# Optimization experiments

Hardware: AMD Instinct MI355X
Metric: run time of the kernel (lower is better)

## Reference

```python
import jax, jax.numpy as jnp
import numpy as np

B, N, NF, H = 16, 128, 128, 128


def setup_inputs() -> dict:
    key = jax.random.key(0)
    ks = jax.random.split(key, 10)
    s = lambda k, sh: jax.random.normal(k, sh, dtype=jnp.float32) * (1.0 / np.sqrt(sh[0]))
    return {
        "node_feat": jax.random.normal(ks[0], (B, N, NF), dtype=jnp.float32),
        "pos": jax.random.normal(ks[1], (B, N, 3), dtype=jnp.float32),
        "valid": jnp.ones((B, N), dtype=jnp.float32),
        "adj": jax.random.uniform(ks[2], (B, N, N), dtype=jnp.float32),
        "We1": s(ks[3], (2 * NF + 2, H)),
        "We2": s(ks[4], (H, H)),
        "Wc1": s(ks[5], (H, H)),
        "Wc2": s(ks[6], (H, 1)),
        "Wn1": s(ks[7], (NF + H, H)),
        "Wn2": s(ks[8], (H, NF)),
        "Wi": s(ks[9], (H, 1)),
    }


def reference(node_feat, pos, valid, adj, We1, We2, Wc1, Wc2, Wn1, Wn2, Wi):
    silu = jax.nn.silu
    n = node_feat.shape[1]
    # all-pairs broadcast features [B,N,N,NF]
    hi = jnp.broadcast_to(node_feat[:, :, None, :], (B, n, n, NF))
    hj = jnp.broadcast_to(node_feat[:, None, :, :], (B, n, n, NF))
    vec = pos[:, :, None, :] - pos[:, None, :, :]            # [B,N,N,3]
    dist = jnp.sum(vec * vec, axis=-1, keepdims=True)        # [B,N,N,1]
    adj4 = adj[..., None]                                    # [B,N,N,1]
    edge_input = jnp.concatenate([hi, hj, dist, adj4], axis=-1)
    m_ij = silu(silu(edge_input @ We1) @ We2)                # [B,N,N,H]
    # normalized direction vectors
    norm = jnp.linalg.norm(vec, axis=-1, keepdims=True)
    vecn = vec / jnp.maximum(norm, 1e-10)
    # pairwise valid mask [B,N,N,1]
    vmask = (valid[:, :, None] * valid[:, None, :])[..., None]
    # coordinate update
    C = (1.0 / (jnp.sum(valid, axis=-1) - 1.0))[:, None, None]
    phi_x = silu(m_ij @ Wc1) @ Wc2                           # [B,N,N,1]
    pos_new = pos + C * jnp.sum(vecn * phi_x * vmask, axis=2)
    # inference gating
    e_ij = jax.nn.sigmoid(m_ij @ Wi)
    m_ij = m_ij * e_ij
    # masked message aggregation over j
    message = jnp.sum(m_ij * adj4, axis=2)                   # [B,N,H]
    node_input = jnp.concatenate([node_feat, message], axis=-1)
    node_new = node_feat + silu(node_input @ Wn1) @ Wn2
    return node_new, pos_new
```

## Files before the change

### kernel.cpp

```cpp
#include <hip/hip_runtime.h>
#include <hip/hip_bf16.h>

#define B_  16
#define N_  128
#define NF_ 128
#define H_  128

typedef __attribute__((ext_vector_type(8))) short short8;
typedef __attribute__((ext_vector_type(4))) float floatx4;

__device__ __forceinline__ float silu_f(float x) {
    return x * __builtin_amdgcn_rcpf(1.0f + __expf(-x));
}
__device__ __forceinline__ float sigm_f(float x) {
    return __builtin_amdgcn_rcpf(1.0f + __expf(-x));
}
__device__ __forceinline__ unsigned short f2bf(float x) {
    union { float f; unsigned u; } v; v.f = x;
    unsigned r = (v.u + 0x7FFFu + ((v.u >> 16) & 1u)) >> 16;
    return (unsigned short)r;
}
__device__ __forceinline__ short f2bf_fast(float x) {
    union { __hip_bfloat16 h; short s; } u;
    u.h = __float2bfloat16(x);
    return u.s;
}
__device__ __forceinline__ float bf2f(unsigned short s) {
    union { unsigned u; float f; } v; v.u = ((unsigned)s) << 16;
    return v.f;
}

__global__ __launch_bounds__(128) void k1_pre(const float* __restrict__ nf,
                                              const float* __restrict__ We1,
                                              float* __restrict__ A_ws,
                                              float* __restrict__ Bm_ws) {
    const int b  = blockIdx.x >> 4;
    const int r0 = (blockIdx.x & 15) << 3;
    const int h  = threadIdx.x;
    __shared__ float rows[8][128];
#pragma unroll
    for (int r = 0; r < 8; ++r)
        rows[r][h] = nf[((size_t)(b * N_ + r0 + r)) * NF_ + h];
    __syncthreads();
    float a[8], bm[8];
#pragma unroll
    for (int r = 0; r < 8; ++r) { a[r] = 0.f; bm[r] = 0.f; }
    for (int c = 0; c < NF_; ++c) {
        const float w1 = We1[c * H_ + h];
        const float w2 = We1[(NF_ + c) * H_ + h];
#pragma unroll
        for (int r = 0; r < 8; ++r) {
            const float x = rows[r][c];
            a[r]  = fmaf(x, w1, a[r]);
            bm[r] = fmaf(x, w2, bm[r]);
        }
    }
#pragma unroll
    for (int r = 0; r < 8; ++r) {
        A_ws [((size_t)(b * N_ + r0 + r)) * H_ + h] = a[r];
        Bm_ws[((size_t)(b * N_ + r0 + r)) * H_ + h] = bm[r];
    }
}

__global__ __launch_bounds__(64) void kC(const float* __restrict__ valid,
                                         float* __restrict__ Cinv) {
    const int b = blockIdx.x;
    const int t = threadIdx.x;
    float v = valid[b * N_ + t] + valid[b * N_ + 64 + t];
#pragma unroll
    for (int m = 32; m >= 1; m >>= 1) v += __shfl_down(v, m, 64);
    if (t == 0) Cinv[b] = 1.0f / (v - 1.0f);
}

#define OFF_BM    0
#define OFF_W2T   34816
#define OFF_WC1X  69632
#define OFF_MB    108800
#define OFF_AW    143616
#define OFF_WAB   145792
#define OFF_WC2   146336
#define OFF_POSJ  146848
#define OFF_VALJ  148384
#define OFF_POSI  148896
#define OFF_VALI  149024
#define SMEM_K2   149088

__global__ __launch_bounds__(512, 2) void k2_edge(
        const float* __restrict__ pos,
        const float* __restrict__ valid,
        const float* __restrict__ adj,
        const float* __restrict__ We1,
        const float* __restrict__ We2,
        const float* __restrict__ Wc1,
        const float* __restrict__ Wc2,
        const float* __restrict__ Wi,
        const float* __restrict__ A_ws,
        const float* __restrict__ Bm_ws,
        const float* __restrict__ Cinv,
        float* __restrict__ msg_ws,
        float* __restrict__ pos_out) {
    __shared__ __align__(16) char smem[SMEM_K2];
    unsigned short* BM   = (unsigned short*)(smem + OFF_BM);
    unsigned short* W2T  = (unsigned short*)(smem + OFF_W2T);
    unsigned short* WC1X = (unsigned short*)(smem + OFF_WC1X);
    unsigned short* MB   = (unsigned short*)(smem + OFF_MB);
    unsigned short* AW   = (unsigned short*)(smem + OFF_AW);
    unsigned short* WAB  = (unsigned short*)(smem + OFF_WAB);
    float* wc2s = (float*)(smem + OFF_WC2);
    float* posj = (float*)(smem + OFF_POSJ);
    float* valj = (float*)(smem + OFF_VALJ);
    float* posi = (float*)(smem + OFF_POSI);
    float* vali = (float*)(smem + OFF_VALI);

    const int tid = threadIdx.x;
    const int b   = blockIdx.x >> 4;
    const int i0  = (blockIdx.x & 15) << 3;

    for (int q = tid; q < (N_ * H_) / 4; q += 512) {
        const int j  = q >> 5;
        const int ch = (q << 2) & 127;
        const float4 v = *(const float4*)(Bm_ws + ((size_t)(b * N_ + j)) * H_ + ch);
        ushort4 o;
        o.x = f2bf(v.x); o.y = f2bf(v.y); o.z = f2bf(v.z); o.w = f2bf(v.w);
        *(ushort4*)(BM + j * 136 + ch) = o;
    }
    for (int x = tid; x < H_ * H_; x += 512) {
        const int k = x >> 7, n = x & 127;
        W2T[n * 136 + k] = f2bf(We2[x]);
    }
    for (int x = tid; x < H_ * H_; x += 512) {
        const int k = x >> 7, n = x & 127;
        WC1X[n * 136 + k] = f2bf(Wc1[x]);
    }
    if (tid < 128) WC1X[128 * 136 + tid] = f2bf(Wi[tid]);
    for (int x = tid; x < 15 * 136; x += 512)
        WC1X[129 * 136 + x] = 0;
    for (int x = tid; x < 8 * H_; x += 512)
        AW[(x >> 7) * 136 + (x & 127)] =
            f2bf(A_ws[((size_t)(b * N_ + i0 + (x >> 7))) * H_ + (x & 127)]);
    if (tid < 256)
        WAB[(tid >> 7) * 136 + (tid & 127)] = f2bf(We1[(256 + (tid >> 7)) * H_ + (tid & 127)]);
    if (tid < 128) {
        wc2s[tid] = Wc2[tid];
        valj[tid] = valid[b * N_ + tid];
    }
    if (tid >= 128) posj[tid - 128] = pos[b * N_ * 3 + (tid - 128)];
    if (tid < 24)   posi[tid] = pos[b * N_ * 3 + i0 * 3 + tid];
    if (tid >= 32 && tid < 40) vali[tid - 32] = valid[b * N_ + i0 + (tid - 32)];
    __syncthreads();

    const int w  = tid >> 6;
    const int l  = tid & 63;
    const int lr = l & 15;
    const int lg = l >> 4;
    const int i  = i0 + w;
    unsigned short* MBs = MB + w * (16 * 136);

    float wc2v[8];
#pragma unroll
    for (int nt = 0; nt < 8; ++nt) wc2v[nt] = wc2s[nt * 16 + lr];
    const float vi   = vali[w];
    const float pix  = posi[w * 3 + 0], piy = posi[w * 3 + 1], piz = posi[w * 3 + 2];
    const float cinv = Cinv[b];

    float msg[8] = {0.f, 0.f, 0.f, 0.f, 0.f, 0.f, 0.f, 0.f};
    float px = 0.f, py = 0.f, pz = 0.f;
    const floatx4 zf = {0.f, 0.f, 0.f, 0.f};

    for (int jc = 0; jc < 8; ++jc) {
        const int jj = jc * 16 + lr;
        const float adjv = adj[((size_t)(b * N_ + i)) * N_ + jj];
        const float vj   = valj[jj];
        const float vx = pix - posj[jj * 3 + 0];
        const float vy = piy - posj[jj * 3 + 1];
        const float vz = piz - posj[jj * 3 + 2];
        const float dist = vx * vx + vy * vy + vz * vz;
        const float vm   = vi * vj;
        const float rn   = __builtin_amdgcn_rcpf(fmaxf(sqrtf(dist), 1e-10f));
        const float vnx = vx * rn, vny = vy * rn, vnz = vz * rn;

        short8 af[4];
#pragma unroll
        for (int ks = 0; ks < 4; ++ks) {
            const int co = ks * 32 + lg * 8;
            const short8 bm8 = *(const short8*)(BM + jj * 136 + co);
            const short8 aw8 = *(const short8*)(AW + w * 136 + co);
            const short8 wa8 = *(const short8*)(WAB + co);
            const short8 wb8 = *(const short8*)(WAB + 136 + co);
#pragma unroll
            for (int e = 0; e < 8; ++e) {
                const float pre = bf2f((unsigned short)aw8[e])
                                + bf2f((unsigned short)bm8[e])
                                + dist * bf2f((unsigned short)wa8[e])
                                + adjv * bf2f((unsigned short)wb8[e]);
                af[ks][e] = f2bf_fast(silu_f(pre));
            }
        }
        floatx4 acc1[8];
#pragma unroll
        for (int nt = 0; nt < 8; ++nt) acc1[nt] = zf;
#pragma unroll
        for (int nt = 0; nt < 8; ++nt)
#pragma unroll
            for (int ks = 0; ks < 4; ++ks) {
                const short8 bf = *(const short8*)(W2T + (nt * 16 + lr) * 136 + ks * 32 + lg * 8);
                acc1[nt] = __builtin_amdgcn_mfma_f32_16x16x32_bf16(af[ks], bf, acc1[nt], 0, 0, 0);
            }
#pragma unroll
        for (int nt = 0; nt < 8; ++nt)
#pragma unroll
            for (int r = 0; r < 4; ++r)
                acc1[nt][r] = silu_f(acc1[nt][r]);

#pragma unroll
        for (int nt = 0; nt < 8; ++nt)
#pragma unroll
            for (int r = 0; r < 4; ++r)
                MBs[(lg * 4 + r) * 136 + nt * 16 + lr] = (unsigned short)f2bf_fast(acc1[nt][r]);
        short8 af2[4];
#pragma unroll
        for (int ks = 0; ks < 4; ++ks)
            af2[ks] = *(const short8*)(MBs + lr * 136 + ks * 32 + lg * 8);

        floatx4 accg = zf;
#pragma unroll
        for (int ks = 0; ks < 4; ++ks) {
            const short8 bf = *(const short8*)(WC1X + (8 * 16 + lr) * 136 + ks * 32 + lg * 8);
            accg = __builtin_amdgcn_mfma_f32_16x16x32_bf16(af2[ks], bf, accg, 0, 0, 0);
        }
        float t4[4];
#pragma unroll
        for (int r = 0; r < 4; ++r) {
            const float ep  = __shfl(accg[r], l & 48);
            const float ajr = __shfl(adjv, (l & 48) | (lg * 4 + r));
            t4[r] = sigm_f(ep) * ajr;
        }
#pragma unroll
        for (int nt = 0; nt < 8; ++nt)
            msg[nt] += acc1[nt][0] * t4[0] + acc1[nt][1] * t4[1]
                     + acc1[nt][2] * t4[2] + acc1[nt][3] * t4[3];

        float ph[4] = {0.f, 0.f, 0.f, 0.f};
#pragma unroll
        for (int nt = 0; nt < 8; ++nt) {
            floatx4 acc2 = zf;
#pragma unroll
            for (int ks = 0; ks < 4; ++ks) {
                const short8 bf = *(const short8*)(WC1X + (nt * 16 + lr) * 136 + ks * 32 + lg * 8);
                acc2 = __builtin_amdgcn_mfma_f32_16x16x32_bf16(af2[ks], bf, acc2, 0, 0, 0);
            }
#pragma unroll
            for (int r = 0; r < 4; ++r)
                ph[r] = fmaf(silu_f(acc2[r]), wc2v[nt], ph[r]);
        }
#pragma unroll
        for (int msk = 1; msk <= 8; msk <<= 1)
#pragma unroll
            for (int r = 0; r < 4; ++r)
                ph[r] += __shfl_xor(ph[r], msk);
        const int src = ((lr >> 2) << 4) | lr;
        const float q0 = __shfl(ph[0], src), q1 = __shfl(ph[1], src);
        const float q2 = __shfl(ph[2], src), q3 = __shfl(ph[3], src);
        const int rr = lr & 3;
        const float phl = rr == 0 ? q0 : rr == 1 ? q1 : rr == 2 ? q2 : q3;
        const float pm = phl * vm;
        px = fmaf(vnx, pm, px); py = fmaf(vny, pm, py); pz = fmaf(vnz, pm, pz);
    }

#pragma unroll
    for (int msk = 16; msk <= 32; msk <<= 1)
#pragma unroll
        for (int nt = 0; nt < 8; ++nt)
            msg[nt] += __shfl_xor(msg[nt], msk);
    if (l < 16) {
#pragma unroll
        for (int nt = 0; nt < 8; ++nt)
            msg_ws[((size_t)(b * N_ + i)) * H_ + nt * 16 + l] = msg[nt];
    }
#pragma unroll
    for (int msk = 1; msk <= 8; msk <<= 1) {
        px += __shfl_xor(px, msk);
        py += __shfl_xor(py, msk);
        pz += __shfl_xor(pz, msk);
    }
    if (l == 0) {
        const size_t o = ((size_t)(b * N_ + i)) * 3;
        pos_out[o + 0] = pos[o + 0] + cinv * px;
        pos_out[o + 1] = pos[o + 1] + cinv * py;
        pos_out[o + 2] = pos[o + 2] + cinv * pz;
    }
}

__global__ __launch_bounds__(128) void k3_node(
        const float* __restrict__ nf,
        const float* __restrict__ Wn1,
        const float* __restrict__ Wn2,
        const float* __restrict__ msg_ws,
        float* __restrict__ out) {
    const int b  = blockIdx.x >> 4;
    const int r0 = (blockIdx.x & 15) << 3;
    const int h  = threadIdx.x;
    __shared__ float in_s[8][256];
    __shared__ float t_s[8][128];
#pragma unroll
    for (int r = 0; r < 8; ++r) {
        in_s[r][h]       = nf[((size_t)(b * N_ + r0 + r)) * NF_ + h];
        in_s[r][128 + h] = msg_ws[((size_t)(b * N_ + r0 + r)) * H_ + h];
    }
    __syncthreads();
    float acc[8];
#pragma unroll
    for (int r = 0; r < 8; ++r) acc[r] = 0.f;
    for (int c = 0; c < 256; ++c) {
        const float wv = Wn1[c * H_ + h];
#pragma unroll
        for (int r = 0; r < 8; ++r) acc[r] = fmaf(in_s[r][c], wv, acc[r]);
    }
#pragma unroll
    for (int r = 0; r < 8; ++r) t_s[r][h] = silu_f(acc[r]);
    __syncthreads();
    float o[8];
#pragma unroll
    for (int r = 0; r < 8; ++r) o[r] = 0.f;
    for (int c = 0; c < 128; ++c) {
        const float wv = Wn2[c * NF_ + h];
#pragma unroll
        for (int r = 0; r < 8; ++r) o[r] = fmaf(t_s[r][c], wv, o[r]);
    }
#pragma unroll
    for (int r = 0; r < 8; ++r)
        out[((size_t)(b * N_ + r0 + r)) * NF_ + h] = in_s[r][h] + o[r];
}

extern "C" void kernel_launch(void* const* d_in, const int* in_sizes, int n_in,
                              void* d_out, int out_size, void* d_ws, size_t ws_size,
                              hipStream_t stream) {
    const float* node_feat = (const float*)d_in[0];
    const float* pos   = (const float*)d_in[1];
    const float* valid = (const float*)d_in[2];
    const float* adj   = (const float*)d_in[3];
    const float* We1   = (const float*)d_in[4];
    const float* We2   = (const float*)d_in[5];
    const float* Wc1   = (const float*)d_in[6];
    const float* Wc2   = (const float*)d_in[7];
    const float* Wn1   = (const float*)d_in[8];
    const float* Wn2   = (const float*)d_in[9];
    const float* Wi    = (const float*)d_in[10];

    float* out     = (float*)d_out;
    float* pos_out = out + (size_t)B_ * N_ * NF_;

    const size_t node_elems = (size_t)B_ * N_ * H_;
    if (ws_size < (3 * node_elems + B_) * sizeof(float)) return;
    float* A_ws   = (float*)d_ws;
    float* Bm_ws  = A_ws + node_elems;
    float* msg_ws = Bm_ws + node_elems;
    float* Cinv   = msg_ws + node_elems;

    k1_pre<<<B_ * 16, 128, 0, stream>>>(node_feat, We1, A_ws, Bm_ws);
    kC<<<B_, 64, 0, stream>>>(valid, Cinv);
    k2_edge<<<B_ * 16, 512, 0, stream>>>(pos, valid, adj, We1, We2, Wc1, Wc2, Wi,
                                         A_ws, Bm_ws, Cinv, msg_ws, pos_out);
    k3_node<<<B_ * 16, 128, 0, stream>>>(node_feat, Wn1, Wn2, msg_ws, out);
}
```

Baseline: 82.78 us.

## Shrink edge-kernel LDS with XOR swizzle, bf16 Bm from global, scalar gate

k1 now writes Bm directly as bf16, and k2 reads it from global memory instead of staging a padded copy in LDS. The weight tiles switch from padded rows to an XOR-swizzled layout, and the per-wave scratch buffer is cut to one 16x32 slice. The Wi gate is computed with a cross-lane reduction instead of an extra MFMA column. Together these shrink LDS from about 149KB to 80KB, so launch bounds can ask for 4 blocks per CU instead of 2. The cost is global-memory loads of Bm in the inner loop and tighter register limits.

```diff
diff --git a/kernel.cpp b/kernel.cpp
--- a/kernel.cpp
+++ b/kernel.cpp
@@ -33,7 +33,7 @@
 __global__ __launch_bounds__(128) void k1_pre(const float* __restrict__ nf,
                                               const float* __restrict__ We1,
                                               float* __restrict__ A_ws,
-                                              float* __restrict__ Bm_ws) {
+                                              unsigned short* __restrict__ Bmh) {
     const int b  = blockIdx.x >> 4;
     const int r0 = (blockIdx.x & 15) << 3;
     const int h  = threadIdx.x;
@@ -57,8 +57,8 @@
     }
 #pragma unroll
     for (int r = 0; r < 8; ++r) {
-        A_ws [((size_t)(b * N_ + r0 + r)) * H_ + h] = a[r];
-        Bm_ws[((size_t)(b * N_ + r0 + r)) * H_ + h] = bm[r];
+        A_ws[((size_t)(b * N_ + r0 + r)) * H_ + h] = a[r];
+        Bmh [((size_t)(b * N_ + r0 + r)) * H_ + h] = f2bf(bm[r]);
     }
 }
 
@@ -72,20 +72,20 @@
     if (t == 0) Cinv[b] = 1.0f / (v - 1.0f);
 }
 
-#define OFF_BM    0
-#define OFF_W2T   34816
-#define OFF_WC1X  69632
-#define OFF_MB    108800
-#define OFF_AW    143616
-#define OFF_WAB   145792
-#define OFF_WC2   146336
-#define OFF_POSJ  146848
-#define OFF_VALJ  148384
-#define OFF_POSI  148896
-#define OFF_VALI  149024
-#define SMEM_K2   149088
-
-__global__ __launch_bounds__(512, 2) void k2_edge(
+#define OFF_W2T   0
+#define OFF_WC1T  32768
+#define OFF_MB    65536
+#define OFF_AW    73728
+#define OFF_WAB   75776
+#define OFF_WC2   76288
+#define OFF_WIS   76800
+#define OFF_POSJ  77312
+#define OFF_VALJ  78848
+#define OFF_POSI  79360
+#define OFF_VALI  79488
+#define SMEM_K2   79552
+
+__global__ __launch_bounds__(512, 4) void k2_edge(
         const float* __restrict__ pos,
         const float* __restrict__ valid,
         const float* __restrict__ adj,
@@ -95,18 +95,18 @@
         const float* __restrict__ Wc2,
         const float* __restrict__ Wi,
         const float* __restrict__ A_ws,
-        const float* __restrict__ Bm_ws,
+        const unsigned short* __restrict__ Bmh,
         const float* __restrict__ Cinv,
         float* __restrict__ msg_ws,
         float* __restrict__ pos_out) {
     __shared__ __align__(16) char smem[SMEM_K2];
-    unsigned short* BM   = (unsigned short*)(smem + OFF_BM);
-    unsigned short* W2T  = (unsigned short*)(smem + OFF_W2T);
-    unsigned short* WC1X = (unsigned short*)(smem + OFF_WC1X);
-    unsigned short* MB   = (unsigned short*)(smem + OFF_MB);
-    unsigned short* AW   = (unsigned short*)(smem + OFF_AW);
-    unsigned short* WAB  = (unsigned short*)(smem + OFF_WAB);
+    char* W2Tb  = smem + OFF_W2T;
+    char* WC1Tb = smem + OFF_WC1T;
+    unsigned short* MB  = (unsigned short*)(smem + OFF_MB);
+    unsigned short* AW  = (unsigned short*)(smem + OFF_AW);
+    unsigned short* WAB = (unsigned short*)(smem + OFF_WAB);
     float* wc2s = (float*)(smem + OFF_WC2);
+    float* wis  = (float*)(smem + OFF_WIS);
     float* posj = (float*)(smem + OFF_POSJ);
     float* valj = (float*)(smem + OFF_VALJ);
     float* posi = (float*)(smem + OFF_POSI);
@@ -116,32 +116,22 @@
     const int b   = blockIdx.x >> 4;
     const int i0  = (blockIdx.x & 15) << 3;
 
-    for (int q = tid; q < (N_ * H_) / 4; q += 512) {
-        const int j  = q >> 5;
-        const int ch = (q << 2) & 127;
-        const float4 v = *(const float4*)(Bm_ws + ((size_t)(b * N_ + j)) * H_ + ch);
-        ushort4 o;
-        o.x = f2bf(v.x); o.y = f2bf(v.y); o.z = f2bf(v.z); o.w = f2bf(v.w);
-        *(ushort4*)(BM + j * 136 + ch) = o;
-    }
     for (int x = tid; x < H_ * H_; x += 512) {
         const int k = x >> 7, n = x & 127;
-        W2T[n * 136 + k] = f2bf(We2[x]);
+        *(unsigned short*)(W2Tb + ((n * 256 + k * 2) ^ ((n & 7) << 4))) = f2bf(We2[x]);
     }
     for (int x = tid; x < H_ * H_; x += 512) {
         const int k = x >> 7, n = x & 127;
-        WC1X[n * 136 + k] = f2bf(Wc1[x]);
-    }
-    if (tid < 128) WC1X[128 * 136 + tid] = f2bf(Wi[tid]);
-    for (int x = tid; x < 15 * 136; x += 512)
-        WC1X[129 * 136 + x] = 0;
+        *(unsigned short*)(WC1Tb + ((n * 256 + k * 2) ^ ((n & 7) << 4))) = f2bf(Wc1[x]);
+    }
     for (int x = tid; x < 8 * H_; x += 512)
-        AW[(x >> 7) * 136 + (x & 127)] =
+        AW[(x >> 7) * 128 + (x & 127)] =
             f2bf(A_ws[((size_t)(b * N_ + i0 + (x >> 7))) * H_ + (x & 127)]);
     if (tid < 256)
-        WAB[(tid >> 7) * 136 + (tid & 127)] = f2bf(We1[(256 + (tid >> 7)) * H_ + (tid & 127)]);
+        WAB[(tid >> 7) * 128 + (tid & 127)] = f2bf(We1[(256 + (tid >> 7)) * H_ + (tid & 127)]);
     if (tid < 128) {
         wc2s[tid] = Wc2[tid];
+        wis[tid]  = Wi[tid];
         valj[tid] = valid[b * N_ + tid];
     }
     if (tid >= 128) posj[tid - 128] = pos[b * N_ * 3 + (tid - 128)];
@@ -154,11 +144,13 @@
     const int lr = l & 15;
     const int lg = l >> 4;
     const int i  = i0 + w;
-    unsigned short* MBs = MB + w * (16 * 136);
-
-    float wc2v[8];
-#pragma unroll
-    for (int nt = 0; nt < 8; ++nt) wc2v[nt] = wc2s[nt * 16 + lr];
+    unsigned short* MBq = MB + w * 512;
+
+    const int swv = (lr & 7) << 4;
+    int cs[4];
+#pragma unroll
+    for (int ks = 0; ks < 4; ++ks) cs[ks] = (ks * 64 + lg * 16) ^ swv;
+
     const float vi   = vali[w];
     const float pix  = posi[w * 3 + 0], piy = posi[w * 3 + 1], piz = posi[w * 3 + 2];
     const float cinv = Cinv[b];
@@ -183,10 +175,10 @@
 #pragma unroll
         for (int ks = 0; ks < 4; ++ks) {
             const int co = ks * 32 + lg * 8;
-            const short8 bm8 = *(const short8*)(BM + jj * 136 + co);
-            const short8 aw8 = *(const short8*)(AW + w * 136 + co);
+            const short8 bm8 = *(const short8*)(Bmh + ((size_t)(b * N_ + jj)) * H_ + co);
+            const short8 aw8 = *(const short8*)(AW + w * 128 + co);
             const short8 wa8 = *(const short8*)(WAB + co);
-            const short8 wb8 = *(const short8*)(WAB + 136 + co);
+            const short8 wb8 = *(const short8*)(WAB + 128 + co);
 #pragma unroll
             for (int e = 0; e < 8; ++e) {
                 const float pre = bf2f((unsigned short)aw8[e])
@@ -203,7 +195,7 @@
         for (int nt = 0; nt < 8; ++nt)
 #pragma unroll
             for (int ks = 0; ks < 4; ++ks) {
-                const short8 bf = *(const short8*)(W2T + (nt * 16 + lr) * 136 + ks * 32 + lg * 8);
+                const short8 bf = *(const short8*)(W2Tb + (nt * 16 + lr) * 256 + cs[ks]);
                 acc1[nt] = __builtin_amdgcn_mfma_f32_16x16x32_bf16(af[ks], bf, acc1[nt], 0, 0, 0);
             }
 #pragma unroll
@@ -212,46 +204,57 @@
             for (int r = 0; r < 4; ++r)
                 acc1[nt][r] = silu_f(acc1[nt][r]);
 
-#pragma unroll
-        for (int nt = 0; nt < 8; ++nt)
-#pragma unroll
-            for (int r = 0; r < 4; ++r)
-                MBs[(lg * 4 + r) * 136 + nt * 16 + lr] = (unsigned short)f2bf_fast(acc1[nt][r]);
-        short8 af2[4];
-#pragma unroll
-        for (int ks = 0; ks < 4; ++ks)
-            af2[ks] = *(const short8*)(MBs + lr * 136 + ks * 32 + lg * 8);
-
-        floatx4 accg = zf;
-#pragma unroll
-        for (int ks = 0; ks < 4; ++ks) {
-            const short8 bf = *(const short8*)(WC1X + (8 * 16 + lr) * 136 + ks * 32 + lg * 8);
-            accg = __builtin_amdgcn_mfma_f32_16x16x32_bf16(af2[ks], bf, accg, 0, 0, 0);
-        }
+        float ep[4] = {0.f, 0.f, 0.f, 0.f};
+#pragma unroll
+        for (int nt = 0; nt < 8; ++nt) {
+            const float wv = wis[nt * 16 + lr];
+#pragma unroll
+            for (int r = 0; r < 4; ++r)
+                ep[r] = fmaf(acc1[nt][r], wv, ep[r]);
+        }
+#pragma unroll
+        for (int msk = 1; msk <= 8; msk <<= 1)
+#pragma unroll
+            for (int r = 0; r < 4; ++r)
+                ep[r] += __shfl_xor(ep[r], msk);
         float t4[4];
 #pragma unroll
         for (int r = 0; r < 4; ++r) {
-            const float ep  = __shfl(accg[r], l & 48);
             const float ajr = __shfl(adjv, (l & 48) | (lg * 4 + r));
-            t4[r] = sigm_f(ep) * ajr;
+            t4[r] = sigm_f(ep[r]) * ajr;
         }
 #pragma unroll
         for (int nt = 0; nt < 8; ++nt)
             msg[nt] += acc1[nt][0] * t4[0] + acc1[nt][1] * t4[1]
                      + acc1[nt][2] * t4[2] + acc1[nt][3] * t4[3];
 
+        short8 af2[4];
+#pragma unroll
+        for (int ks = 0; ks < 4; ++ks) {
+#pragma unroll
+            for (int h = 0; h < 2; ++h) {
+                const int nt = 2 * ks + h;
+#pragma unroll
+                for (int r = 0; r < 4; ++r)
+                    MBq[(lg * 4 + r) * 32 + h * 16 + lr] =
+                        (unsigned short)f2bf_fast(acc1[nt][r]);
+            }
+            af2[ks] = *(const short8*)(MBq + lr * 32 + lg * 8);
+        }
+
         float ph[4] = {0.f, 0.f, 0.f, 0.f};
 #pragma unroll
         for (int nt = 0; nt < 8; ++nt) {
             floatx4 acc2 = zf;
 #pragma unroll
             for (int ks = 0; ks < 4; ++ks) {
-                const short8 bf = *(const short8*)(WC1X + (nt * 16 + lr) * 136 + ks * 32 + lg * 8);
+                const short8 bf = *(const short8*)(WC1Tb + (nt * 16 + lr) * 256 + cs[ks]);
                 acc2 = __builtin_amdgcn_mfma_f32_16x16x32_bf16(af2[ks], bf, acc2, 0, 0, 0);
             }
-#pragma unroll
-            for (int r = 0; r < 4; ++r)
-                ph[r] = fmaf(silu_f(acc2[r]), wc2v[nt], ph[r]);
+            const float wv = wc2s[nt * 16 + lr];
+#pragma unroll
+            for (int r = 0; r < 4; ++r)
+                ph[r] = fmaf(silu_f(acc2[r]), wv, ph[r]);
         }
 #pragma unroll
         for (int msk = 1; msk <= 8; msk <<= 1)
@@ -351,15 +354,15 @@
     float* pos_out = out + (size_t)B_ * N_ * NF_;
 
     const size_t node_elems = (size_t)B_ * N_ * H_;
-    if (ws_size < (3 * node_elems + B_) * sizeof(float)) return;
-    float* A_ws   = (float*)d_ws;
-    float* Bm_ws  = A_ws + node_elems;
-    float* msg_ws = Bm_ws + node_elems;
+    if (ws_size < node_elems * 4 + node_elems * 2 + node_elems * 4 + 64) return;
+    float* A_ws = (float*)d_ws;
+    unsigned short* Bmh = (unsigned short*)(A_ws + node_elems);
+    float* msg_ws = (float*)((char*)Bmh + node_elems * 2);
     float* Cinv   = msg_ws + node_elems;
 
-    k1_pre<<<B_ * 16, 128, 0, stream>>>(node_feat, We1, A_ws, Bm_ws);
+    k1_pre<<<B_ * 16, 128, 0, stream>>>(node_feat, We1, A_ws, Bmh);
     kC<<<B_, 64, 0, stream>>>(valid, Cinv);
     k2_edge<<<B_ * 16, 512, 0, stream>>>(pos, valid, adj, We1, We2, Wc1, Wc2, Wi,
-                                         A_ws, Bm_ws, Cinv, msg_ws, pos_out);
+                                         A_ws, Bmh, Cinv, msg_ws, pos_out);
     k3_node<<<B_ * 16, 128, 0, stream>>>(node_feat, Wn1, Wn2, msg_ws, out);
 }
```

Result: slower. 95.65 us (+15.5%).

## Split edge j-loop across two waves per row and shrink staging buffer

Applied to the files above, without the earlier changes.

The edge kernel now launches 1024 threads per block, with two waves per node row each handling half of the j chunks. Partial messages and position updates are combined through shared memory after a block barrier. The per-wave staging buffer is cut to a 16x32 slice that is reused per k-step, which lowers LDS use. This doubles the waves available to hide MFMA and memory latency but adds a reduction step and a barrier, and the launch bounds put heavy pressure on registers.

```diff
diff --git a/kernel.cpp b/kernel.cpp
--- a/kernel.cpp
+++ b/kernel.cpp
@@ -75,17 +75,19 @@
 #define OFF_BM    0
 #define OFF_W2T   34816
 #define OFF_WC1X  69632
-#define OFF_MB    108800
-#define OFF_AW    143616
-#define OFF_WAB   145792
-#define OFF_WC2   146336
-#define OFF_POSJ  146848
-#define OFF_VALJ  148384
-#define OFF_POSI  148896
-#define OFF_VALI  149024
-#define SMEM_K2   149088
-
-__global__ __launch_bounds__(512, 2) void k2_edge(
+#define OFF_MBQ   108800
+#define OFF_AW    125184
+#define OFF_WAB   127360
+#define OFF_WC2   127904
+#define OFF_POSJ  128416
+#define OFF_VALJ  129952
+#define OFF_POSI  130464
+#define OFF_VALI  130592
+#define OFF_MSGC  130656
+#define OFF_POSC  138848
+#define SMEM_K2   139104
+
+__global__ __launch_bounds__(1024, 4) void k2_edge(
         const float* __restrict__ pos,
         const float* __restrict__ valid,
         const float* __restrict__ adj,
@@ -103,7 +105,7 @@
     unsigned short* BM   = (unsigned short*)(smem + OFF_BM);
     unsigned short* W2T  = (unsigned short*)(smem + OFF_W2T);
     unsigned short* WC1X = (unsigned short*)(smem + OFF_WC1X);
-    unsigned short* MB   = (unsigned short*)(smem + OFF_MB);
+    unsigned short* MBQ  = (unsigned short*)(smem + OFF_MBQ);
     unsigned short* AW   = (unsigned short*)(smem + OFF_AW);
     unsigned short* WAB  = (unsigned short*)(smem + OFF_WAB);
     float* wc2s = (float*)(smem + OFF_WC2);
@@ -111,12 +113,14 @@
     float* valj = (float*)(smem + OFF_VALJ);
     float* posi = (float*)(smem + OFF_POSI);
     float* vali = (float*)(smem + OFF_VALI);
+    float* MSGC = (float*)(smem + OFF_MSGC);
+    float* POSC = (float*)(smem + OFF_POSC);
 
     const int tid = threadIdx.x;
     const int b   = blockIdx.x >> 4;
     const int i0  = (blockIdx.x & 15) << 3;
 
-    for (int q = tid; q < (N_ * H_) / 4; q += 512) {
+    for (int q = tid; q < (N_ * H_) / 4; q += 1024) {
         const int j  = q >> 5;
         const int ch = (q << 2) & 127;
         const float4 v = *(const float4*)(Bm_ws + ((size_t)(b * N_ + j)) * H_ + ch);
@@ -124,50 +128,51 @@
         o.x = f2bf(v.x); o.y = f2bf(v.y); o.z = f2bf(v.z); o.w = f2bf(v.w);
         *(ushort4*)(BM + j * 136 + ch) = o;
     }
-    for (int x = tid; x < H_ * H_; x += 512) {
+    for (int x = tid; x < H_ * H_; x += 1024) {
         const int k = x >> 7, n = x & 127;
         W2T[n * 136 + k] = f2bf(We2[x]);
     }
-    for (int x = tid; x < H_ * H_; x += 512) {
+    for (int x = tid; x < H_ * H_; x += 1024) {
         const int k = x >> 7, n = x & 127;
         WC1X[n * 136 + k] = f2bf(Wc1[x]);
     }
     if (tid < 128) WC1X[128 * 136 + tid] = f2bf(Wi[tid]);
-    for (int x = tid; x < 15 * 136; x += 512)
+    for (int x = tid; x < 15 * 136; x += 1024)
         WC1X[129 * 136 + x] = 0;
-    for (int x = tid; x < 8 * H_; x += 512)
-        AW[(x >> 7) * 136 + (x & 127)] =
-            f2bf(A_ws[((size_t)(b * N_ + i0 + (x >> 7))) * H_ + (x & 127)]);
+    AW[(tid >> 7) * 136 + (tid & 127)] =
+        f2bf(A_ws[((size_t)(b * N_ + i0 + (tid >> 7))) * H_ + (tid & 127)]);
     if (tid < 256)
         WAB[(tid >> 7) * 136 + (tid & 127)] = f2bf(We1[(256 + (tid >> 7)) * H_ + (tid & 127)]);
     if (tid < 128) {
         wc2s[tid] = Wc2[tid];
         valj[tid] = valid[b * N_ + tid];
     }
-    if (tid >= 128) posj[tid - 128] = pos[b * N_ * 3 + (tid - 128)];
+    if (tid >= 128 && tid < 512) posj[tid - 128] = pos[b * N_ * 3 + (tid - 128)];
     if (tid < 24)   posi[tid] = pos[b * N_ * 3 + i0 * 3 + tid];
     if (tid >= 32 && tid < 40) vali[tid - 32] = valid[b * N_ + i0 + (tid - 32)];
     __syncthreads();
 
-    const int w  = tid >> 6;
-    const int l  = tid & 63;
-    const int lr = l & 15;
-    const int lg = l >> 4;
-    const int i  = i0 + w;
-    unsigned short* MBs = MB + w * (16 * 136);
+    const int w    = tid >> 6;
+    const int row  = w >> 1;
+    const int half = w & 1;
+    const int l    = tid & 63;
+    const int lr   = l & 15;
+    const int lg   = l >> 4;
+    const int i    = i0 + row;
+    unsigned short* MBq = MBQ + w * 512;
 
     float wc2v[8];
 #pragma unroll
     for (int nt = 0; nt < 8; ++nt) wc2v[nt] = wc2s[nt * 16 + lr];
-    const float vi   = vali[w];
-    const float pix  = posi[w * 3 + 0], piy = posi[w * 3 + 1], piz = posi[w * 3 + 2];
+    const float vi   = vali[row];
+    const float pix  = posi[row * 3 + 0], piy = posi[row * 3 + 1], piz = posi[row * 3 + 2];
     const float cinv = Cinv[b];
 
     float msg[8] = {0.f, 0.f, 0.f, 0.f, 0.f, 0.f, 0.f, 0.f};
     float px = 0.f, py = 0.f, pz = 0.f;
     const floatx4 zf = {0.f, 0.f, 0.f, 0.f};
 
-    for (int jc = 0; jc < 8; ++jc) {
+    for (int jc = half * 4; jc < half * 4 + 4; ++jc) {
         const int jj = jc * 16 + lr;
         const float adjv = adj[((size_t)(b * N_ + i)) * N_ + jj];
         const float vj   = valj[jj];
@@ -184,7 +189,7 @@
         for (int ks = 0; ks < 4; ++ks) {
             const int co = ks * 32 + lg * 8;
             const short8 bm8 = *(const short8*)(BM + jj * 136 + co);
-            const short8 aw8 = *(const short8*)(AW + w * 136 + co);
+            const short8 aw8 = *(const short8*)(AW + row * 136 + co);
             const short8 wa8 = *(const short8*)(WAB + co);
             const short8 wb8 = *(const short8*)(WAB + 136 + co);
 #pragma unroll
@@ -212,15 +217,19 @@
             for (int r = 0; r < 4; ++r)
                 acc1[nt][r] = silu_f(acc1[nt][r]);
 
-#pragma unroll
-        for (int nt = 0; nt < 8; ++nt)
-#pragma unroll
-            for (int r = 0; r < 4; ++r)
-                MBs[(lg * 4 + r) * 136 + nt * 16 + lr] = (unsigned short)f2bf_fast(acc1[nt][r]);
         short8 af2[4];
 #pragma unroll
-        for (int ks = 0; ks < 4; ++ks)
-            af2[ks] = *(const short8*)(MBs + lr * 136 + ks * 32 + lg * 8);
+        for (int ks = 0; ks < 4; ++ks) {
+#pragma unroll
+            for (int h = 0; h < 2; ++h) {
+                const int nt = 2 * ks + h;
+#pragma unroll
+                for (int r = 0; r < 4; ++r)
+                    MBq[(lg * 4 + r) * 32 + h * 16 + lr] =
+                        (unsigned short)f2bf_fast(acc1[nt][r]);
+            }
+            af2[ks] = *(const short8*)(MBq + lr * 32 + lg * 8);
+        }
 
         floatx4 accg = zf;
 #pragma unroll
@@ -275,7 +284,7 @@
     if (l < 16) {
 #pragma unroll
         for (int nt = 0; nt < 8; ++nt)
-            msg_ws[((size_t)(b * N_ + i)) * H_ + nt * 16 + l] = msg[nt];
+            MSGC[(half * 8 + row) * 128 + nt * 16 + l] = msg[nt];
     }
 #pragma unroll
     for (int msk = 1; msk <= 8; msk <<= 1) {
@@ -284,10 +293,20 @@
         pz += __shfl_xor(pz, msk);
     }
     if (l == 0) {
-        const size_t o = ((size_t)(b * N_ + i)) * 3;
-        pos_out[o + 0] = pos[o + 0] + cinv * px;
-        pos_out[o + 1] = pos[o + 1] + cinv * py;
-        pos_out[o + 2] = pos[o + 2] + cinv * pz;
+        POSC[(half * 8 + row) * 3 + 0] = px;
+        POSC[(half * 8 + row) * 3 + 1] = py;
+        POSC[(half * 8 + row) * 3 + 2] = pz;
+    }
+    __syncthreads();
+    {
+        const int r2 = tid >> 7, ch = tid & 127;
+        msg_ws[((size_t)(b * N_ + i0 + r2)) * H_ + ch] =
+            MSGC[r2 * 128 + ch] + MSGC[(8 + r2) * 128 + ch];
+    }
+    if (tid < 24) {
+        const int r2 = tid / 3, c = tid % 3;
+        const size_t o = ((size_t)(b * N_ + i0 + r2)) * 3 + c;
+        pos_out[o] = pos[o] + cinv * (POSC[r2 * 3 + c] + POSC[(8 + r2) * 3 + c]);
     }
 }
 
@@ -359,7 +378,7 @@
 
     k1_pre<<<B_ * 16, 128, 0, stream>>>(node_feat, We1, A_ws, Bm_ws);
     kC<<<B_, 64, 0, stream>>>(valid, Cinv);
-    k2_edge<<<B_ * 16, 512, 0, stream>>>(pos, valid, adj, We1, We2, Wc1, Wc2, Wi,
-                                         A_ws, Bm_ws, Cinv, msg_ws, pos_out);
+    k2_edge<<<B_ * 16, 1024, 0, stream>>>(pos, valid, adj, We1, We2, Wc1, Wc2, Wi,
+                                          A_ws, Bm_ws, Cinv, msg_ws, pos_out);
     k3_node<<<B_ * 16, 128, 0, stream>>>(node_feat, Wn1, Wn2, msg_ws, out);
 }
```

Result: slower. 94.69 us (+14.4%).
